# Kernel optimization log

Measured on AMD Instinct MI355X. Metric: run time of the kernel, lower is better.

Reference implementation:

```python
import jax, jax.numpy as jnp
import numpy as np

B, N, D, H, K, FFN = 8, 256, 512, 16, 4, 2048
DK = D // H
NEG = -1e12


def _lin(k, i, o):
    return jax.random.normal(k, (i, o), jnp.float32) / np.sqrt(i)


def setup_inputs() -> dict:
    key = jax.random.key(0)
    ks = jax.random.split(key, 12)
    return {
        "x": jax.random.normal(ks[0], (B, N, D), jnp.float32),
        "dist": jax.random.uniform(ks[1], (B, N - 1, N - 1), jnp.float32) * 10.0,
        "dist_bar": jnp.array([1.5, 3.0, 5.0, 8.0], jnp.float32),
        "attn_bias": 0.1 * jax.random.normal(ks[2], (B, K, N, N), jnp.float32),
        "mask": jnp.ones((B, 1, N, N), jnp.int32),
        "num_heads": H,
        "Wq": _lin(ks[3], D, D), "bq": jnp.zeros((D,), jnp.float32),
        "Wk": _lin(ks[4], D, D), "bk": jnp.zeros((D,), jnp.float32),
        "Wv": _lin(ks[5], D, D), "bv": jnp.zeros((D,), jnp.float32),
        "W1": _lin(ks[6], K * D, D), "b1": jnp.zeros((D,), jnp.float32),
        "W2": _lin(ks[7], D, D), "b2": jnp.zeros((D,), jnp.float32),
        "g1": jnp.ones((D,), jnp.float32), "be1": jnp.zeros((D,), jnp.float32),
        "Wf1": _lin(ks[8], D, FFN), "bf1": jnp.zeros((FFN,), jnp.float32),
        "Wf2": _lin(ks[9], FFN, D), "bf2": jnp.zeros((D,), jnp.float32),
        "g2": jnp.ones((D,), jnp.float32), "be2": jnp.zeros((D,), jnp.float32),
    }


def _ln(x, g, b, eps=1e-6):
    m = jnp.mean(x, -1, keepdims=True)
    v = jnp.mean((x - m) ** 2, -1, keepdims=True)
    return (x - m) / jnp.sqrt(v + eps) * g + b


def _forward(x, dist, dist_bar, attn_bias, mask, num_heads,
             Wq, bq, Wk, bk, Wv, bv, W1, b1, W2, b2, g1, be1,
             Wf1, bf1, Wf2, bf2, g2, be2):
    Bn, Nn, Dn = x.shape
    Hh = num_heads
    dk = Dn // Hh
    Kk = dist_bar.shape[0]

    q = (x @ Wq + bq).reshape(Bn, Nn, Hh, dk).transpose(0, 2, 1, 3)  # [B,H,N,dk]
    k = (x @ Wk + bk).reshape(Bn, Nn, Hh, dk).transpose(0, 2, 1, 3)
    v = (x @ Wv + bv).reshape(Bn, Nn, Hh, dk).transpose(0, 2, 1, 3)

    scores = jnp.einsum('bhnd,bhmd->bhnm', q, k) / np.sqrt(dk)      # [B,H,N,N]
    # expand over scales and add bias: [B,H,K,N,N]
    scores = scores[:, :, None, :, :] + attn_bias[:, None, :, :, :]
    # padding mask [B,1,N,N] -> broadcast over H,K
    scores = jnp.where(mask[:, None] == 0, NEG, scores)

    # build padded distance with super node (row/col 0 distance = 0)
    nd = jnp.ones((Bn, Nn, Nn), x.dtype)
    nd = nd.at[:, 1:, 1:].set(dist)
    nd = nd.at[:, 0, :].set(0.0).at[:, :, 0].set(0.0)
    masks = nd[:, None, None, :, :] < dist_bar.reshape(1, 1, Kk, 1, 1)  # [B,1,K,N,N]
    masks = masks.at[:, :, :, 0, :].set(True).at[:, :, :, :, 0].set(True)

    scores = jnp.where(masks, scores, NEG)
    attn = jax.nn.softmax(scores, axis=-1)                           # [B,H,K,N,N]

    msg = jnp.einsum('bhknm,bhmd->bhknd', attn, v)                   # [B,H,K,N,dk]
    # faithful to torch: transpose(1,2).view(B,H*K,N,dk) then transpose(2,3).view(B,N,-1)
    msg = jnp.transpose(msg, (0, 2, 1, 3, 4)).reshape(Bn, Kk * Hh, Nn, dk)
    msg = jnp.transpose(msg, (0, 1, 3, 2)).reshape(Bn, Nn, Kk * Hh * dk)

    h = jax.nn.silu(msg @ W1 + b1) @ W2 + b2
    y = _ln(h + x, g1, be1)

    f = jax.nn.gelu(y @ Wf1 + bf1, approximate=False) @ Wf2 + bf2
    out = _ln(f + y, g2, be2)
    return out


def reference(x, dist, dist_bar, attn_bias, mask, num_heads,
              Wq, bq, Wk, bk, Wv, bv, W1, b1, W2, b2, g1, be1,
              Wf1, bf1, Wf2, bf2, g2, be2):
    return _forward(x, dist, dist_bar, attn_bias, mask, num_heads,
                    Wq, bq, Wk, bk, Wv, bv, W1, b1, W2, b2, g1, be1,
                    Wf1, bf1, Wf2, bf2, g2, be2)
```

## Files before the change

### kernel.cpp

```cpp
#include <hip/hip_runtime.h>
#include <math.h>

#define BB 8
#define NN 256
#define DD 512
#define HH 16
#define KK 4
#define DKK 32
#define FFN_ 2048
#define NEGV -1e12f

typedef __attribute__((ext_vector_type(8))) short bf16x8;
typedef __attribute__((ext_vector_type(4))) float f32x4;

__device__ __forceinline__ unsigned short f2bf(float f) {
    union { float f; unsigned int u; } v; v.f = f;
    unsigned int r = (v.u + 0x7FFFu + ((v.u >> 16) & 1u)) >> 16;
    return (unsigned short)r;
}
__device__ __forceinline__ float bf2f(unsigned short u) {
    union { unsigned int i; float f; } v; v.i = ((unsigned int)u) << 16;
    return v.f;
}
__device__ __forceinline__ void gload_lds16(const unsigned short* g, unsigned short* l) {
    __builtin_amdgcn_global_load_lds(
        (const __attribute__((address_space(1))) void*)g,
        (__attribute__((address_space(3))) void*)l, 16, 0, 0);
}

__global__ __launch_bounds__(256) void prep_kernel(
    const float* __restrict__ x,
    const float* __restrict__ Wq, const float* __restrict__ Wk,
    const float* __restrict__ Wv, const float* __restrict__ W1,
    const float* __restrict__ W2, const float* __restrict__ Wf1,
    const float* __restrict__ Wf2,
    const float* __restrict__ bq, const float* __restrict__ bk,
    const float* __restrict__ bv,
    const float* __restrict__ attn_bias, const int* __restrict__ mask,
    const float* __restrict__ dist, const float* __restrict__ dist_bar,
    unsigned short* __restrict__ xb, unsigned short* __restrict__ Wqkvt,
    unsigned short* __restrict__ W1t, unsigned short* __restrict__ W2t,
    unsigned short* __restrict__ Wf1t, unsigned short* __restrict__ Wf2t,
    float* __restrict__ bqkv, unsigned short* __restrict__ biasMs)
{
    const int z = blockIdx.z;
    const int t = threadIdx.x;

    if (z == 7) {
        if (blockIdx.x >= 1024) return;
        const int i0 = blockIdx.x * 1024 + t * 4;
        float4 xv = *(const float4*)(x + i0);
        ushort4 o;
        o.x = f2bf(xv.x); o.y = f2bf(xv.y); o.z = f2bf(xv.z); o.w = f2bf(xv.w);
        *(ushort4*)(xb + i0) = o;
        return;
    }
    if (z == 8) {
        if (blockIdx.x >= 6) return;
        const int i = blockIdx.x * 256 + t;
        float v = (i < 512) ? bq[i] : (i < 1024) ? bk[i - 512] : bv[i - 1024];
        bqkv[i] = v;
        return;
    }
    if (z == 9) {
        const int bx = blockIdx.x;
        const int rg = bx & 63, ks = (bx >> 6) & 3, b = bx >> 8;
        const int m = t;
        const float bar = dist_bar[ks];
        ushort4 o;
        unsigned short* po = (unsigned short*)&o;
        #pragma unroll
        for (int i = 0; i < 4; ++i) {
            const int n = rg * 4 + i;
            const int mk = mask[((size_t)(b * NN) + n) * NN + m];
            bool allowed = (n == 0) || (m == 0);
            if (!allowed)
                allowed = dist[((size_t)(b * 255) + (n - 1)) * 255 + (m - 1)] < bar;
            const float bias = attn_bias[(((size_t)(b * KK) + ks) * NN + n) * NN + m];
            po[i] = f2bf((mk != 0 && allowed) ? bias : NEGV);
        }
        *(ushort4*)(biasMs + (size_t)bx * 1024 + m * 4) = o;
        return;
    }

    const float* src; unsigned short* dst; int Kd, Nd;
    switch (z) {
        case 0: src = Wq;  dst = Wqkvt;              Kd = 512;  Nd = 512;  break;
        case 1: src = Wk;  dst = Wqkvt + 512 * 512;  Kd = 512;  Nd = 512;  break;
        case 2: src = Wv;  dst = Wqkvt + 1024 * 512; Kd = 512;  Nd = 512;  break;
        case 3: src = W1;  dst = W1t;  Kd = 2048; Nd = 512;  break;
        case 4: src = W2;  dst = W2t;  Kd = 512;  Nd = 512;  break;
        case 5: src = Wf1; dst = Wf1t; Kd = 512;  Nd = 2048; break;
        default: src = Wf2; dst = Wf2t; Kd = 2048; Nd = 512; break;
    }
    const int ktiles = Kd / 32, ntiles = Nd / 32;
    const int ti = blockIdx.x;
    if (ti >= ktiles * ntiles) return;
    const int k0 = (ti % ktiles) * 32, n0 = (ti / ktiles) * 32;

    __shared__ float tile[32][33];
    const int xx = t & 31, yy = t >> 5;
    #pragma unroll
    for (int r = 0; r < 4; ++r)
        tile[yy * 4 + r][xx] = src[(size_t)(k0 + yy * 4 + r) * Nd + n0 + xx];
    __syncthreads();
    #pragma unroll
    for (int r = 0; r < 4; ++r)
        dst[(size_t)(n0 + yy * 4 + r) * Kd + k0 + xx] = f2bf(tile[xx][yy * 4 + r]);
}

template<int ACT, int EPI, int KSPLIT>
__global__ __launch_bounds__(512) void mfma_gemm512(
    const unsigned short* __restrict__ A, const unsigned short* __restrict__ Bt,
    const float* __restrict__ bias, unsigned short* __restrict__ Cb,
    unsigned short* __restrict__ vT, float* __restrict__ Cp,
    int M, int N, int Kdim)
{
    __shared__ unsigned short As[128 * 64];
    __shared__ unsigned short Bs[128 * 64];

    const int t = threadIdx.x, lane = t & 63, wv = t >> 6;
    const int n0 = blockIdx.x * 128, m0 = blockIdx.y * 128;
    const int wm = wv >> 1, wn = wv & 1;
    const int L = lane & 15, qd = lane >> 4;
    const int sr = lane >> 3, sc = lane & 7;

    const int ksub = Kdim / KSPLIT;
    const int kbeg = blockIdx.z * ksub;

    f32x4 acc[2][4];
    #pragma unroll
    for (int i = 0; i < 2; ++i)
        #pragma unroll
        for (int j = 0; j < 4; ++j) acc[i][j] = (f32x4){0.f, 0.f, 0.f, 0.f};

    for (int kt = kbeg; kt < kbeg + ksub; kt += 64) {
        #pragma unroll
        for (int p = 0; p < 2; ++p) {
            const int rbase = wv * 16 + p * 8;
            gload_lds16(A  + (size_t)(m0 + rbase + sr) * Kdim + kt + sc * 8,
                        As + rbase * 64);
            gload_lds16(Bt + (size_t)(n0 + rbase + sr) * Kdim + kt + sc * 8,
                        Bs + rbase * 64);
        }
        __syncthreads();
        #pragma unroll
        for (int s = 0; s < 2; ++s) {
            bf16x8 af[2], bfb[4];
            #pragma unroll
            for (int i = 0; i < 2; ++i)
                af[i] = *(const bf16x8*)(As + (wm * 32 + i * 16 + L) * 64 + s * 32 + qd * 8);
            #pragma unroll
            for (int j = 0; j < 4; ++j)
                bfb[j] = *(const bf16x8*)(Bs + (wn * 64 + j * 16 + L) * 64 + s * 32 + qd * 8);
            #pragma unroll
            for (int i = 0; i < 2; ++i)
                #pragma unroll
                for (int j = 0; j < 4; ++j)
                    acc[i][j] = __builtin_amdgcn_mfma_f32_16x16x32_bf16(af[i], bfb[j], acc[i][j], 0, 0, 0);
        }
        __syncthreads();
    }

    #pragma unroll
    for (int j = 0; j < 4; ++j) {
        const int col = n0 + wn * 64 + j * 16 + L;
        #pragma unroll
        for (int i = 0; i < 2; ++i) {
            const int rowb = m0 + wm * 32 + i * 16 + qd * 4;
            if (EPI == 2) {
                float* cp = Cp + (size_t)blockIdx.z * M * N + (size_t)rowb * N + col;
                #pragma unroll
                for (int r = 0; r < 4; ++r) cp[(size_t)r * N] = acc[i][j][r];
            } else if (EPI == 1 && col >= 1024) {
                const float bv = bias[col];
                ushort4 pk;
                unsigned short* pp = (unsigned short*)&pk;
                #pragma unroll
                for (int r = 0; r < 4; ++r) pp[r] = f2bf(acc[i][j][r] + bv);
                *(ushort4*)(vT + (size_t)(col - 1024) * 2048 + rowb) = pk;
            } else {
                const float bv = bias[col];
                #pragma unroll
                for (int r = 0; r < 4; ++r) {
                    float v = acc[i][j][r] + bv;
                    if (ACT == 1) v = v / (1.0f + __expf(-v));
                    else if (ACT == 2) v = 0.5f * v * (1.0f + erff(v * 0.70710678118654752f));
                    Cb[(size_t)(rowb + r) * N + col] = f2bf(v);
                }
            }
        }
    }
}

__global__ __launch_bounds__(256) void fin_silu(
    const float* __restrict__ Cp, const float* __restrict__ bias,
    unsigned short* __restrict__ out)
{
    const int row = blockIdx.x, t = threadIdx.x;
    const int c0 = t * 2;
    const size_t base = (size_t)row * DD;
    float sx = 0.f, sy = 0.f;
    #pragma unroll
    for (int z = 0; z < 4; ++z) {
        const float2 p = *(const float2*)(Cp + (size_t)z * (2048u * 512u) + base + c0);
        sx += p.x; sy += p.y;
    }
    float v0 = sx + bias[c0], v1 = sy + bias[c0 + 1];
    v0 = v0 / (1.0f + __expf(-v0));
    v1 = v1 / (1.0f + __expf(-v1));
    ushort2 pk; pk.x = f2bf(v0); pk.y = f2bf(v1);
    *(ushort2*)(out + base + c0) = pk;
}

template<int KS, int OUT16>
__global__ __launch_bounds__(256) void fin_ln(
    const float* __restrict__ Cp, const float* __restrict__ bias,
    const float* __restrict__ res, const float* __restrict__ g,
    const float* __restrict__ be, float* __restrict__ out,
    unsigned short* __restrict__ outb)
{
    const int row = blockIdx.x, t = threadIdx.x;
    const int c0 = t * 2;
    const size_t base = (size_t)row * DD;
    __shared__ float red[256];

    float sx = 0.f, sy = 0.f;
    #pragma unroll
    for (int z = 0; z < KS; ++z) {
        const float2 p = *(const float2*)(Cp + (size_t)z * (2048u * 512u) + base + c0);
        sx += p.x; sy += p.y;
    }
    const float2 rv = *(const float2*)(res + base + c0);
    const float z0 = sx + bias[c0]     + rv.x;
    const float z1 = sy + bias[c0 + 1] + rv.y;

    red[t] = z0 + z1; __syncthreads();
    for (int s = 128; s > 0; s >>= 1) {
        if (t < s) red[t] += red[t + s];
        __syncthreads();
    }
    const float mean = red[0] * (1.0f / 512.0f); __syncthreads();

    const float d0 = z0 - mean, d1 = z1 - mean;
    red[t] = d0 * d0 + d1 * d1; __syncthreads();
    for (int s = 128; s > 0; s >>= 1) {
        if (t < s) red[t] += red[t + s];
        __syncthreads();
    }
    const float inv = rsqrtf(red[0] * (1.0f / 512.0f) + 1e-6f);

    const float o0 = d0 * inv * g[c0]     + be[c0];
    const float o1 = d1 * inv * g[c0 + 1] + be[c0 + 1];
    out[base + c0]     = o0;
    out[base + c0 + 1] = o1;
    if (OUT16) {
        ushort2 pk; pk.x = f2bf(o0); pk.y = f2bf(o1);
        *(ushort2*)(outb + base + c0) = pk;
    }
}

__global__ __launch_bounds__(256) void attn_kernel(
    const unsigned short* __restrict__ qkvb, const unsigned short* __restrict__ vT,
    const unsigned short* __restrict__ biasMs, unsigned short* __restrict__ msgT)
{
    const int qt = blockIdx.x, h = blockIdx.y, b = blockIdx.z;
    const int q0 = qt * 64;
    const int t = threadIdx.x, lane = t & 63, wv = t >> 6;
    const int L = lane & 15, qd = lane >> 4;

    __shared__ unsigned short Qs[64 * 32];
    __shared__ unsigned short Ks[256 * 32];
    __shared__ unsigned short Vs[32 * 264];
    __shared__ unsigned short Ps[64 * 264];
    __shared__ unsigned short Ot[32 * 72];

    {
        const int r = lane >> 2, c = lane & 3;
        gload_lds16(qkvb + (size_t)(b * NN + q0 + wv * 16 + r) * 1536 + h * DKK + c * 8,
                    Qs + wv * 16 * 32);
        #pragma unroll
        for (int p = 0; p < 4; ++p)
            gload_lds16(qkvb + (size_t)(b * NN + p * 64 + wv * 16 + r) * 1536 + 512 + h * DKK + c * 8,
                        Ks + (p * 64 + wv * 16) * 32);
    }
    {
        const int vr = t >> 3, seg = t & 7;
        const unsigned short* gv = vT + (size_t)(h * DKK + vr) * 2048 + b * NN + seg * 32;
        #pragma unroll
        for (int i = 0; i < 4; ++i) {
            bf16x8 vv = *(const bf16x8*)(gv + i * 8);
            *(bf16x8*)(Vs + vr * 264 + seg * 32 + i * 8) = vv;
        }
    }
    __syncthreads();

    f32x4 S[16];
    #pragma unroll
    for (int j = 0; j < 16; ++j) S[j] = (f32x4){0.f, 0.f, 0.f, 0.f};
    {
        const bf16x8 aq = *(const bf16x8*)(Qs + (wv * 16 + L) * 32 + qd * 8);
        #pragma unroll
        for (int j = 0; j < 16; ++j) {
            const bf16x8 bk = *(const bf16x8*)(Ks + (j * 16 + L) * 32 + qd * 8);
            S[j] = __builtin_amdgcn_mfma_f32_16x16x32_bf16(aq, bk, S[j], 0, 0, 0);
        }
    }
    const float scale = 0.17677669529663687f;
    const int rgb = (q0 + wv * 16) >> 2;

    for (int ks = 0; ks < KK; ++ks) {
        const unsigned short* bp = biasMs + ((size_t)((b * KK + ks) * 64 + rgb + qd)) * 1024;

        ushort4 b4[16];
        float mx[4] = {-3e38f, -3e38f, -3e38f, -3e38f};
        #pragma unroll
        for (int j = 0; j < 16; ++j) {
            b4[j] = *(const ushort4*)(bp + (j * 16 + L) * 4);
            const unsigned short* pb = (const unsigned short*)&b4[j];
            #pragma unroll
            for (int r = 0; r < 4; ++r)
                mx[r] = fmaxf(mx[r], S[j][r] * scale + bf2f(pb[r]));
        }
        #pragma unroll
        for (int off = 8; off > 0; off >>= 1)
            #pragma unroll
            for (int r = 0; r < 4; ++r)
                mx[r] = fmaxf(mx[r], __shfl_xor(mx[r], off));

        float sm[4] = {0.f, 0.f, 0.f, 0.f};
        #pragma unroll
        for (int j = 0; j < 16; ++j) {
            const unsigned short* pb = (const unsigned short*)&b4[j];
            #pragma unroll
            for (int r = 0; r < 4; ++r) {
                const float e = __expf(S[j][r] * scale + bf2f(pb[r]) - mx[r]);
                sm[r] += e;
                Ps[(wv * 16 + qd * 4 + r) * 264 + j * 16 + L] = f2bf(e);
            }
        }
        #pragma unroll
        for (int off = 8; off > 0; off >>= 1)
            #pragma unroll
            for (int r = 0; r < 4; ++r)
                sm[r] += __shfl_xor(sm[r], off);
        float inv[4];
        #pragma unroll
        for (int r = 0; r < 4; ++r) inv[r] = 1.0f / sm[r];

        f32x4 O[2];
        O[0] = (f32x4){0.f, 0.f, 0.f, 0.f};
        O[1] = (f32x4){0.f, 0.f, 0.f, 0.f};
        #pragma unroll
        for (int kc = 0; kc < 8; ++kc) {
            const bf16x8 ap = *(const bf16x8*)(Ps + (wv * 16 + L) * 264 + kc * 32 + qd * 8);
            #pragma unroll
            for (int jt = 0; jt < 2; ++jt) {
                const bf16x8 bv = *(const bf16x8*)(Vs + (jt * 16 + L) * 264 + kc * 32 + qd * 8);
                O[jt] = __builtin_amdgcn_mfma_f32_16x16x32_bf16(ap, bv, O[jt], 0, 0, 0);
            }
        }
        #pragma unroll
        for (int jt = 0; jt < 2; ++jt)
            #pragma unroll
            for (int r = 0; r < 4; ++r)
                Ot[(jt * 16 + L) * 72 + wv * 16 + qd * 4 + r] = f2bf(O[jt][r] * inv[r]);
        __syncthreads();

        {
            const int dd = t >> 3, cc = t & 7;
            bf16x8 ov = *(const bf16x8*)(Ot + dd * 72 + cc * 8);
            *(bf16x8*)(msgT + (size_t)b * 524288 +
                       ((size_t)((ks * HH + h) * DKK + dd)) * NN + q0 + cc * 8) = ov;
        }
        __syncthreads();
    }
}

extern "C" void kernel_launch(void* const* d_in, const int* in_sizes, int n_in,
                              void* d_out, int out_size, void* d_ws, size_t ws_size,
                              hipStream_t stream)
{
    const float* x         = (const float*)d_in[0];
    const float* dist      = (const float*)d_in[1];
    const float* dist_bar  = (const float*)d_in[2];
    const float* attn_bias = (const float*)d_in[3];
    const int*   mask      = (const int*)d_in[4];
    const float* Wq  = (const float*)d_in[6];  const float* bq  = (const float*)d_in[7];
    const float* Wk  = (const float*)d_in[8];  const float* bk  = (const float*)d_in[9];
    const float* Wv  = (const float*)d_in[10]; const float* bv  = (const float*)d_in[11];
    const float* W1  = (const float*)d_in[12]; const float* b1  = (const float*)d_in[13];
    const float* W2  = (const float*)d_in[14]; const float* b2  = (const float*)d_in[15];
    const float* g1  = (const float*)d_in[16]; const float* be1 = (const float*)d_in[17];
    const float* Wf1 = (const float*)d_in[18]; const float* bf1 = (const float*)d_in[19];
    const float* Wf2 = (const float*)d_in[20]; const float* bf2 = (const float*)d_in[21];
    const float* g2  = (const float*)d_in[22]; const float* be2 = (const float*)d_in[23];

    float* ws = (float*)d_ws;
    unsigned short* qkvb   = (unsigned short*)(ws + 0);
    unsigned short* vT     = (unsigned short*)(ws + 1572864);
    unsigned short* xb     = (unsigned short*)(ws + 2097152);
    unsigned short* msgT   = (unsigned short*)(ws + 2621440);
    unsigned short* g3     = msgT;
    unsigned short* biasMs = (unsigned short*)(ws + 4718592);
    float*          bqkv   = ws + 5767168;
    unsigned short* h1     = (unsigned short*)(ws + 5771264);
    float*          yb     = ws + 6295552;
    unsigned short* yb16   = (unsigned short*)(ws + 7344128);
    unsigned short* Wqkvt  = (unsigned short*)(ws + 7868416);
    unsigned short* W1t    = (unsigned short*)(ws + 8261632);
    unsigned short* W2t    = (unsigned short*)(ws + 8785920);
    unsigned short* Wf1t   = (unsigned short*)(ws + 8916992);
    unsigned short* Wf2t   = (unsigned short*)(ws + 9441280);
    float*          part   = ws + 9965568;
    float*          outp   = (float*)d_out;

    const int M = BB * NN;

    prep_kernel<<<dim3(2048, 1, 10), dim3(256), 0, stream>>>(
        x, Wq, Wk, Wv, W1, W2, Wf1, Wf2, bq, bk, bv,
        attn_bias, mask, dist, dist_bar,
        xb, Wqkvt, W1t, W2t, Wf1t, Wf2t, bqkv, biasMs);

    mfma_gemm512<0,1,1><<<dim3(12, 16, 1), dim3(512), 0, stream>>>(
        xb, Wqkvt, bqkv, qkvb, vT, nullptr, M, 1536, DD);

    attn_kernel<<<dim3(4, HH, BB), dim3(256), 0, stream>>>(qkvb, vT, biasMs, msgT);

    mfma_gemm512<0,2,4><<<dim3(4, 16, 4), dim3(512), 0, stream>>>(
        msgT, W1t, nullptr, nullptr, nullptr, part, M, DD, 2048);
    fin_silu<<<dim3(M), dim3(256), 0, stream>>>(part, b1, h1);

    mfma_gemm512<0,2,2><<<dim3(4, 16, 2), dim3(512), 0, stream>>>(
        h1, W2t, nullptr, nullptr, nullptr, part, M, DD, DD);
    fin_ln<2,1><<<dim3(M), dim3(256), 0, stream>>>(part, b2, x, g1, be1, yb, yb16);

    mfma_gemm512<2,0,1><<<dim3(16, 16, 1), dim3(512), 0, stream>>>(
        yb16, Wf1t, bf1, g3, nullptr, nullptr, M, FFN_, DD);

    mfma_gemm512<0,2,4><<<dim3(4, 16, 4), dim3(512), 0, stream>>>(
        g3, Wf2t, nullptr, nullptr, nullptr, part, M, DD, 2048);
    fin_ln<4,0><<<dim3(M), dim3(256), 0, stream>>>(part, bf2, yb, g2, be2, outp, nullptr);
}
```

Baseline: 254.0 us.

## Fuse all stages into one cooperative persistent kernel with grid syncs

Replaces the chain of ten separate kernel launches with a single cooperative mega-kernel of 256 blocks that runs prep, QKV GEMM, attention, the MLP GEMMs and layer norms as stages separated by grid.sync. Split-K partial buffers and finalize kernels are removed: GEMMs now use 64x64 tiles with fused bias/activation epilogues, and layer norm becomes a wave-per-row shuffle reduction. Attention is restructured so each block handles half the queries of one (batch, head), with per-wave scratch. The aim is to cut launch overhead and partial-sum traffic, at the cost of low parallelism in some stages (256 blocks, long-K GEMMs with small tiles) and grid-wide barrier costs.

Result: slower. 529.2 us (+108.3%).

```diff
diff --git a/kernel.cpp b/kernel.cpp
--- a/kernel.cpp
+++ b/kernel.cpp
@@ -1,5 +1,8 @@
 #include <hip/hip_runtime.h>
+#include <hip/hip_cooperative_groups.h>
 #include <math.h>
+
+namespace cg = cooperative_groups;
 
 #define BB 8
 #define NN 256
@@ -28,7 +31,7 @@
         (__attribute__((address_space(3))) void*)l, 16, 0, 0);
 }
 
-__global__ __launch_bounds__(256) void prep_kernel(
+__device__ void prep_stage(
     const float* __restrict__ x,
     const float* __restrict__ Wq, const float* __restrict__ Wk,
     const float* __restrict__ Wv, const float* __restrict__ W1,
@@ -41,92 +44,83 @@
     unsigned short* __restrict__ xb, unsigned short* __restrict__ Wqkvt,
     unsigned short* __restrict__ W1t, unsigned short* __restrict__ W2t,
     unsigned short* __restrict__ Wf1t, unsigned short* __restrict__ Wf2t,
-    float* __restrict__ bqkv, unsigned short* __restrict__ biasMs)
-{
-    const int z = blockIdx.z;
+    float* __restrict__ bqkv, unsigned short* __restrict__ biasMs, char* lds)
+{
+    float* tile = (float*)lds;
     const int t = threadIdx.x;
 
-    if (z == 7) {
-        if (blockIdx.x >= 1024) return;
-        const int i0 = blockIdx.x * 1024 + t * 4;
-        float4 xv = *(const float4*)(x + i0);
-        ushort4 o;
-        o.x = f2bf(xv.x); o.y = f2bf(xv.y); o.z = f2bf(xv.z); o.w = f2bf(xv.w);
-        *(ushort4*)(xb + i0) = o;
-        return;
-    }
-    if (z == 8) {
-        if (blockIdx.x >= 6) return;
-        const int i = blockIdx.x * 256 + t;
-        float v = (i < 512) ? bq[i] : (i < 1024) ? bk[i - 512] : bv[i - 1024];
-        bqkv[i] = v;
-        return;
-    }
-    if (z == 9) {
-        const int bx = blockIdx.x;
-        const int rg = bx & 63, ks = (bx >> 6) & 3, b = bx >> 8;
-        const int m = t;
-        const float bar = dist_bar[ks];
-        ushort4 o;
-        unsigned short* po = (unsigned short*)&o;
-        #pragma unroll
-        for (int i = 0; i < 4; ++i) {
-            const int n = rg * 4 + i;
-            const int mk = mask[((size_t)(b * NN) + n) * NN + m];
-            bool allowed = (n == 0) || (m == 0);
-            if (!allowed)
-                allowed = dist[((size_t)(b * 255) + (n - 1)) * 255 + (m - 1)] < bar;
-            const float bias = attn_bias[(((size_t)(b * KK) + ks) * NN + n) * NN + m];
-            po[i] = f2bf((mk != 0 && allowed) ? bias : NEGV);
-        }
-        *(ushort4*)(biasMs + (size_t)bx * 1024 + m * 4) = o;
-        return;
-    }
-
-    const float* src; unsigned short* dst; int Kd, Nd;
-    switch (z) {
-        case 0: src = Wq;  dst = Wqkvt;              Kd = 512;  Nd = 512;  break;
-        case 1: src = Wk;  dst = Wqkvt + 512 * 512;  Kd = 512;  Nd = 512;  break;
-        case 2: src = Wv;  dst = Wqkvt + 1024 * 512; Kd = 512;  Nd = 512;  break;
-        case 3: src = W1;  dst = W1t;  Kd = 2048; Nd = 512;  break;
-        case 4: src = W2;  dst = W2t;  Kd = 512;  Nd = 512;  break;
-        case 5: src = Wf1; dst = Wf1t; Kd = 512;  Nd = 2048; break;
-        default: src = Wf2; dst = Wf2t; Kd = 2048; Nd = 512; break;
-    }
-    const int ktiles = Kd / 32, ntiles = Nd / 32;
-    const int ti = blockIdx.x;
-    if (ti >= ktiles * ntiles) return;
-    const int k0 = (ti % ktiles) * 32, n0 = (ti / ktiles) * 32;
-
-    __shared__ float tile[32][33];
-    const int xx = t & 31, yy = t >> 5;
-    #pragma unroll
-    for (int r = 0; r < 4; ++r)
-        tile[yy * 4 + r][xx] = src[(size_t)(k0 + yy * 4 + r) * Nd + n0 + xx];
-    __syncthreads();
-    #pragma unroll
-    for (int r = 0; r < 4; ++r)
-        dst[(size_t)(n0 + yy * 4 + r) * Kd + k0 + xx] = f2bf(tile[xx][yy * 4 + r]);
-}
-
-template<int ACT, int EPI, int KSPLIT>
-__global__ __launch_bounds__(512) void mfma_gemm512(
-    const unsigned short* __restrict__ A, const unsigned short* __restrict__ Bt,
-    const float* __restrict__ bias, unsigned short* __restrict__ Cb,
-    unsigned short* __restrict__ vT, float* __restrict__ Cp,
-    int M, int N, int Kdim)
-{
-    __shared__ unsigned short As[128 * 64];
-    __shared__ unsigned short Bs[128 * 64];
-
+    for (int job = blockIdx.x; job < 5379; job += 256) {
+        if (job < 4096) {
+            const float* src; unsigned short* dst; int Kd, Nd, ti;
+            if (job < 768) {
+                const int w = job >> 8; ti = job & 255;
+                src = (w == 0) ? Wq : (w == 1) ? Wk : Wv;
+                dst = Wqkvt + w * 262144; Kd = 512; Nd = 512;
+            } else if (job < 1792) { src = W1;  dst = W1t;  Kd = 2048; Nd = 512;  ti = job - 768; }
+            else if (job < 2048)   { src = W2;  dst = W2t;  Kd = 512;  Nd = 512;  ti = job - 1792; }
+            else if (job < 3072)   { src = Wf1; dst = Wf1t; Kd = 512;  Nd = 2048; ti = job - 2048; }
+            else                   { src = Wf2; dst = Wf2t; Kd = 2048; Nd = 512;  ti = job - 3072; }
+            const int kt = Kd >> 5;
+            const int k0 = (ti % kt) * 32, n0 = (ti / kt) * 32;
+            const int xx = t & 31, yy = t >> 5;
+            __syncthreads();
+            #pragma unroll
+            for (int rr = 0; rr < 2; ++rr)
+                tile[(yy * 2 + rr) * 33 + xx] = src[(size_t)(k0 + yy * 2 + rr) * Nd + n0 + xx];
+            __syncthreads();
+            #pragma unroll
+            for (int rr = 0; rr < 2; ++rr)
+                dst[(size_t)(n0 + yy * 2 + rr) * Kd + k0 + xx] = f2bf(tile[xx * 33 + yy * 2 + rr]);
+        } else if (job < 4352) {
+            const int j = job - 4096;
+            const size_t i0 = (size_t)j * 4096 + t * 8;
+            const float4 a = *(const float4*)(x + i0);
+            const float4 c = *(const float4*)(x + i0 + 4);
+            unsigned short o[8] = {f2bf(a.x), f2bf(a.y), f2bf(a.z), f2bf(a.w),
+                                   f2bf(c.x), f2bf(c.y), f2bf(c.z), f2bf(c.w)};
+            *(bf16x8*)(xb + i0) = *(bf16x8*)o;
+        } else if (job < 5376) {
+            const int j = job - 4352;
+            const int b = j >> 7, ks = (j >> 5) & 3, rgp = j & 31;
+            const int rg = rgp * 2 + (t >> 8), m = t & 255;
+            const int bx = (b * 4 + ks) * 64 + rg;
+            const float bar = dist_bar[ks];
+            ushort4 o; unsigned short* po = (unsigned short*)&o;
+            #pragma unroll
+            for (int i = 0; i < 4; ++i) {
+                const int n = rg * 4 + i;
+                const int mk = mask[((size_t)(b * NN) + n) * NN + m];
+                bool allowed = (n == 0) || (m == 0);
+                if (!allowed)
+                    allowed = dist[((size_t)(b * 255) + (n - 1)) * 255 + (m - 1)] < bar;
+                const float bias = attn_bias[(((size_t)(b * KK) + ks) * NN + n) * NN + m];
+                po[i] = f2bf((mk != 0 && allowed) ? bias : NEGV);
+            }
+            *(ushort4*)(biasMs + (size_t)bx * 1024 + m * 4) = o;
+        } else {
+            const int j = job - 5376;
+            const int i = j * 512 + t;
+            bqkv[i] = (i < 512) ? bq[i] : (i < 1024) ? bk[i - 512] : bv[i - 1024];
+        }
+    }
+}
+
+template<int ACT, int QKV>
+__device__ void gemm128(const unsigned short* __restrict__ A,
+                        const unsigned short* __restrict__ Bt,
+                        const float* __restrict__ bias,
+                        unsigned short* __restrict__ Cb,
+                        unsigned short* __restrict__ vTo,
+                        int N, int Kdim, int njobs, int ntile, char* lds)
+{
+    unsigned short* As = (unsigned short*)lds;
+    unsigned short* Bs = As + 8192;
     const int t = threadIdx.x, lane = t & 63, wv = t >> 6;
-    const int n0 = blockIdx.x * 128, m0 = blockIdx.y * 128;
     const int wm = wv >> 1, wn = wv & 1;
     const int L = lane & 15, qd = lane >> 4;
-    const int sr = lane >> 3, sc = lane & 7;
-
-    const int ksub = Kdim / KSPLIT;
-    const int kbeg = blockIdx.z * ksub;
+    const int job = blockIdx.x;
+    if (job >= njobs) return;
+    const int n0 = (job % ntile) * 128, m0 = (job / ntile) * 128;
 
     f32x4 acc[2][4];
     #pragma unroll
@@ -134,14 +128,13 @@
         #pragma unroll
         for (int j = 0; j < 4; ++j) acc[i][j] = (f32x4){0.f, 0.f, 0.f, 0.f};
 
-    for (int kt = kbeg; kt < kbeg + ksub; kt += 64) {
-        #pragma unroll
-        for (int p = 0; p < 2; ++p) {
-            const int rbase = wv * 16 + p * 8;
-            gload_lds16(A  + (size_t)(m0 + rbase + sr) * Kdim + kt + sc * 8,
-                        As + rbase * 64);
-            gload_lds16(Bt + (size_t)(n0 + rbase + sr) * Kdim + kt + sc * 8,
-                        Bs + rbase * 64);
+    for (int kt = 0; kt < Kdim; kt += 64) {
+        #pragma unroll
+        for (int i = 0; i < 2; ++i) {
+            gload_lds16(A  + (size_t)(m0 + wv * 16 + i * 8 + (lane >> 3)) * Kdim + kt + (lane & 7) * 8,
+                        As + (wv * 16 + i * 8) * 64);
+            gload_lds16(Bt + (size_t)(n0 + wv * 16 + i * 8 + (lane >> 3)) * Kdim + kt + (lane & 7) * 8,
+                        Bs + (wv * 16 + i * 8) * 64);
         }
         __syncthreads();
         #pragma unroll
@@ -165,27 +158,20 @@
     #pragma unroll
     for (int j = 0; j < 4; ++j) {
         const int col = n0 + wn * 64 + j * 16 + L;
+        const float bv = bias[col];
         #pragma unroll
         for (int i = 0; i < 2; ++i) {
             const int rowb = m0 + wm * 32 + i * 16 + qd * 4;
-            if (EPI == 2) {
-                float* cp = Cp + (size_t)blockIdx.z * M * N + (size_t)rowb * N + col;
-                #pragma unroll
-                for (int r = 0; r < 4; ++r) cp[(size_t)r * N] = acc[i][j][r];
-            } else if (EPI == 1 && col >= 1024) {
-                const float bv = bias[col];
-                ushort4 pk;
-                unsigned short* pp = (unsigned short*)&pk;
+            if (QKV == 1 && col >= 1024) {
+                ushort4 pk; unsigned short* pp = (unsigned short*)&pk;
                 #pragma unroll
                 for (int r = 0; r < 4; ++r) pp[r] = f2bf(acc[i][j][r] + bv);
-                *(ushort4*)(vT + (size_t)(col - 1024) * 2048 + rowb) = pk;
+                *(ushort4*)(vTo + (size_t)(col - 1024) * 2048 + rowb) = pk;
             } else {
-                const float bv = bias[col];
                 #pragma unroll
                 for (int r = 0; r < 4; ++r) {
                     float v = acc[i][j][r] + bv;
-                    if (ACT == 1) v = v / (1.0f + __expf(-v));
-                    else if (ACT == 2) v = 0.5f * v * (1.0f + erff(v * 0.70710678118654752f));
+                    if (ACT == 2) v = 0.5f * v * (1.0f + erff(v * 0.70710678118654752f));
                     Cb[(size_t)(rowb + r) * N + col] = f2bf(v);
                 }
             }
@@ -193,105 +179,77 @@
     }
 }
 
-__global__ __launch_bounds__(256) void fin_silu(
-    const float* __restrict__ Cp, const float* __restrict__ bias,
-    unsigned short* __restrict__ out)
-{
-    const int row = blockIdx.x, t = threadIdx.x;
-    const int c0 = t * 2;
-    const size_t base = (size_t)row * DD;
-    float sx = 0.f, sy = 0.f;
-    #pragma unroll
-    for (int z = 0; z < 4; ++z) {
-        const float2 p = *(const float2*)(Cp + (size_t)z * (2048u * 512u) + base + c0);
-        sx += p.x; sy += p.y;
-    }
-    float v0 = sx + bias[c0], v1 = sy + bias[c0 + 1];
-    v0 = v0 / (1.0f + __expf(-v0));
-    v1 = v1 / (1.0f + __expf(-v1));
-    ushort2 pk; pk.x = f2bf(v0); pk.y = f2bf(v1);
-    *(ushort2*)(out + base + c0) = pk;
-}
-
-template<int KS, int OUT16>
-__global__ __launch_bounds__(256) void fin_ln(
-    const float* __restrict__ Cp, const float* __restrict__ bias,
-    const float* __restrict__ res, const float* __restrict__ g,
-    const float* __restrict__ be, float* __restrict__ out,
-    unsigned short* __restrict__ outb)
-{
-    const int row = blockIdx.x, t = threadIdx.x;
-    const int c0 = t * 2;
-    const size_t base = (size_t)row * DD;
-    __shared__ float red[256];
-
-    float sx = 0.f, sy = 0.f;
-    #pragma unroll
-    for (int z = 0; z < KS; ++z) {
-        const float2 p = *(const float2*)(Cp + (size_t)z * (2048u * 512u) + base + c0);
-        sx += p.x; sy += p.y;
-    }
-    const float2 rv = *(const float2*)(res + base + c0);
-    const float z0 = sx + bias[c0]     + rv.x;
-    const float z1 = sy + bias[c0 + 1] + rv.y;
-
-    red[t] = z0 + z1; __syncthreads();
-    for (int s = 128; s > 0; s >>= 1) {
-        if (t < s) red[t] += red[t + s];
+template<int ACT, int OUTF32>
+__device__ void gemm64(const unsigned short* __restrict__ A,
+                       const unsigned short* __restrict__ Bt,
+                       const float* __restrict__ bias,
+                       unsigned short* __restrict__ Cb, float* __restrict__ Cf,
+                       int N, int Kdim, char* lds)
+{
+    unsigned short* As = (unsigned short*)lds;
+    unsigned short* Bs = As + 4096;
+    const int t = threadIdx.x, lane = t & 63, wv = t >> 6;
+    const int wm = wv >> 1, wn = wv & 1;
+    const int L = lane & 15, qd = lane >> 4;
+    const int ntile = N >> 6;
+    const int job = blockIdx.x;
+    const int n0 = (job & (ntile - 1)) * 64, m0 = (job / ntile) * 64;
+
+    f32x4 acc[2] = {(f32x4){0.f,0.f,0.f,0.f}, (f32x4){0.f,0.f,0.f,0.f}};
+
+    for (int kt = 0; kt < Kdim; kt += 64) {
+        gload_lds16(A  + (size_t)(m0 + wv * 8 + (lane >> 3)) * Kdim + kt + (lane & 7) * 8,
+                    As + wv * 8 * 64);
+        gload_lds16(Bt + (size_t)(n0 + wv * 8 + (lane >> 3)) * Kdim + kt + (lane & 7) * 8,
+                    Bs + wv * 8 * 64);
         __syncthreads();
-    }
-    const float mean = red[0] * (1.0f / 512.0f); __syncthreads();
-
-    const float d0 = z0 - mean, d1 = z1 - mean;
-    red[t] = d0 * d0 + d1 * d1; __syncthreads();
-    for (int s = 128; s > 0; s >>= 1) {
-        if (t < s) red[t] += red[t + s];
+        #pragma unroll
+        for (int s = 0; s < 2; ++s) {
+            const bf16x8 a = *(const bf16x8*)(As + (wm * 16 + L) * 64 + s * 32 + qd * 8);
+            #pragma unroll
+            for (int j = 0; j < 2; ++j) {
+                const bf16x8 b = *(const bf16x8*)(Bs + (wn * 32 + j * 16 + L) * 64 + s * 32 + qd * 8);
+                acc[j] = __builtin_amdgcn_mfma_f32_16x16x32_bf16(a, b, acc[j], 0, 0, 0);
+            }
+        }
         __syncthreads();
     }
-    const float inv = rsqrtf(red[0] * (1.0f / 512.0f) + 1e-6f);
-
-    const float o0 = d0 * inv * g[c0]     + be[c0];
-    const float o1 = d1 * inv * g[c0 + 1] + be[c0 + 1];
-    out[base + c0]     = o0;
-    out[base + c0 + 1] = o1;
-    if (OUT16) {
-        ushort2 pk; pk.x = f2bf(o0); pk.y = f2bf(o1);
-        *(ushort2*)(outb + base + c0) = pk;
-    }
-}
-
-__global__ __launch_bounds__(256) void attn_kernel(
-    const unsigned short* __restrict__ qkvb, const unsigned short* __restrict__ vT,
-    const unsigned short* __restrict__ biasMs, unsigned short* __restrict__ msgT)
-{
-    const int qt = blockIdx.x, h = blockIdx.y, b = blockIdx.z;
-    const int q0 = qt * 64;
+
+    #pragma unroll
+    for (int j = 0; j < 2; ++j) {
+        const int col = n0 + wn * 32 + j * 16 + L;
+        const float bv = bias[col];
+        #pragma unroll
+        for (int r = 0; r < 4; ++r) {
+            const int row = m0 + wm * 16 + qd * 4 + r;
+            float v = acc[j][r] + bv;
+            if (ACT == 1) v = v / (1.0f + __expf(-v));
+            if (OUTF32) Cf[(size_t)row * N + col] = v;
+            else        Cb[(size_t)row * N + col] = f2bf(v);
+        }
+    }
+}
+
+__device__ void attn_stage(const unsigned short* __restrict__ qkvb,
+                           const unsigned short* __restrict__ vTb,
+                           const unsigned short* __restrict__ biasMs,
+                           unsigned short* __restrict__ msgT, char* lds)
+{
+    const int bid = blockIdx.x;
+    const int b = bid >> 5, h = (bid >> 1) & 15, qh = bid & 1;
     const int t = threadIdx.x, lane = t & 63, wv = t >> 6;
     const int L = lane & 15, qd = lane >> 4;
-
-    __shared__ unsigned short Qs[64 * 32];
-    __shared__ unsigned short Ks[256 * 32];
-    __shared__ unsigned short Vs[32 * 264];
-    __shared__ unsigned short Ps[64 * 264];
-    __shared__ unsigned short Ot[32 * 72];
+    const int qbase = qh * 128 + wv * 16;
+
+    unsigned short* Vs  = (unsigned short*)lds;
+    unsigned short* Pch = (unsigned short*)(lds + 16896) + wv * 640;
+    unsigned short* Ot  = (unsigned short*)(lds + 27136) + wv * 768;
 
     {
-        const int r = lane >> 2, c = lane & 3;
-        gload_lds16(qkvb + (size_t)(b * NN + q0 + wv * 16 + r) * 1536 + h * DKK + c * 8,
-                    Qs + wv * 16 * 32);
-        #pragma unroll
-        for (int p = 0; p < 4; ++p)
-            gload_lds16(qkvb + (size_t)(b * NN + p * 64 + wv * 16 + r) * 1536 + 512 + h * DKK + c * 8,
-                        Ks + (p * 64 + wv * 16) * 32);
-    }
-    {
-        const int vr = t >> 3, seg = t & 7;
-        const unsigned short* gv = vT + (size_t)(h * DKK + vr) * 2048 + b * NN + seg * 32;
-        #pragma unroll
-        for (int i = 0; i < 4; ++i) {
-            bf16x8 vv = *(const bf16x8*)(gv + i * 8);
-            *(bf16x8*)(Vs + vr * 264 + seg * 32 + i * 8) = vv;
-        }
+        const int d = t >> 4, seg = t & 15;
+        const unsigned short* gv = vTb + (size_t)(h * DKK + d) * 2048 + b * NN + seg * 16;
+        *(bf16x8*)(Vs + d * 264 + seg * 16)     = *(const bf16x8*)(gv);
+        *(bf16x8*)(Vs + d * 264 + seg * 16 + 8) = *(const bf16x8*)(gv + 8);
     }
     __syncthreads();
 
@@ -299,15 +257,19 @@
     #pragma unroll
     for (int j = 0; j < 16; ++j) S[j] = (f32x4){0.f, 0.f, 0.f, 0.f};
     {
-        const bf16x8 aq = *(const bf16x8*)(Qs + (wv * 16 + L) * 32 + qd * 8);
+        const bf16x8 aq = *(const bf16x8*)(qkvb + (size_t)(b * NN + qbase + L) * 1536 + h * DKK + qd * 8);
         #pragma unroll
         for (int j = 0; j < 16; ++j) {
-            const bf16x8 bk = *(const bf16x8*)(Ks + (j * 16 + L) * 32 + qd * 8);
+            const bf16x8 bk = *(const bf16x8*)(qkvb + (size_t)(b * NN + j * 16 + L) * 1536 + 512 + h * DKK + qd * 8);
             S[j] = __builtin_amdgcn_mfma_f32_16x16x32_bf16(aq, bk, S[j], 0, 0, 0);
         }
     }
     const float scale = 0.17677669529663687f;
-    const int rgb = (q0 + wv * 16) >> 2;
+    #pragma unroll
+    for (int j = 0; j < 16; ++j)
+        #pragma unroll
+        for (int r = 0; r < 4; ++r) S[j][r] *= scale;
+    const int rgb = qbase >> 2;
 
     for (int ks = 0; ks < KK; ++ks) {
         const unsigned short* bp = biasMs + ((size_t)((b * KK + ks) * 64 + rgb + qd)) * 1024;
@@ -320,30 +282,30 @@
             const unsigned short* pb = (const unsigned short*)&b4[j];
             #pragma unroll
             for (int r = 0; r < 4; ++r)
-                mx[r] = fmaxf(mx[r], S[j][r] * scale + bf2f(pb[r]));
+                mx[r] = fmaxf(mx[r], S[j][r] + bf2f(pb[r]));
         }
         #pragma unroll
         for (int off = 8; off > 0; off >>= 1)
             #pragma unroll
-            for (int r = 0; r < 4; ++r)
-                mx[r] = fmaxf(mx[r], __shfl_xor(mx[r], off));
-
+            for (int r = 0; r < 4; ++r) mx[r] = fmaxf(mx[r], __shfl_xor(mx[r], off));
+
+        ushort4 e16[16];
         float sm[4] = {0.f, 0.f, 0.f, 0.f};
         #pragma unroll
         for (int j = 0; j < 16; ++j) {
             const unsigned short* pb = (const unsigned short*)&b4[j];
+            unsigned short* pe = (unsigned short*)&e16[j];
             #pragma unroll
             for (int r = 0; r < 4; ++r) {
-                const float e = __expf(S[j][r] * scale + bf2f(pb[r]) - mx[r]);
+                const float e = __expf(S[j][r] + bf2f(pb[r]) - mx[r]);
                 sm[r] += e;
-                Ps[(wv * 16 + qd * 4 + r) * 264 + j * 16 + L] = f2bf(e);
+                pe[r] = f2bf(e);
             }
         }
         #pragma unroll
         for (int off = 8; off > 0; off >>= 1)
             #pragma unroll
-            for (int r = 0; r < 4; ++r)
-                sm[r] += __shfl_xor(sm[r], off);
+            for (int r = 0; r < 4; ++r) sm[r] += __shfl_xor(sm[r], off);
         float inv[4];
         #pragma unroll
         for (int r = 0; r < 4; ++r) inv[r] = 1.0f / sm[r];
@@ -353,28 +315,125 @@
         O[1] = (f32x4){0.f, 0.f, 0.f, 0.f};
         #pragma unroll
         for (int kc = 0; kc < 8; ++kc) {
-            const bf16x8 ap = *(const bf16x8*)(Ps + (wv * 16 + L) * 264 + kc * 32 + qd * 8);
+            #pragma unroll
+            for (int j2 = 0; j2 < 2; ++j2) {
+                const unsigned short* pe = (const unsigned short*)&e16[kc * 2 + j2];
+                #pragma unroll
+                for (int r = 0; r < 4; ++r)
+                    Pch[(qd * 4 + r) * 40 + j2 * 16 + L] = pe[r];
+            }
+            asm volatile("s_waitcnt lgkmcnt(0)" ::: "memory");
+            const bf16x8 ap = *(const bf16x8*)(Pch + L * 40 + qd * 8);
             #pragma unroll
             for (int jt = 0; jt < 2; ++jt) {
                 const bf16x8 bv = *(const bf16x8*)(Vs + (jt * 16 + L) * 264 + kc * 32 + qd * 8);
                 O[jt] = __builtin_amdgcn_mfma_f32_16x16x32_bf16(ap, bv, O[jt], 0, 0, 0);
             }
         }
+
         #pragma unroll
         for (int jt = 0; jt < 2; ++jt)
             #pragma unroll
             for (int r = 0; r < 4; ++r)
-                Ot[(jt * 16 + L) * 72 + wv * 16 + qd * 4 + r] = f2bf(O[jt][r] * inv[r]);
-        __syncthreads();
-
+                Ot[(jt * 16 + L) * 24 + qd * 4 + r] = f2bf(O[jt][r] * inv[r]);
+        asm volatile("s_waitcnt lgkmcnt(0)" ::: "memory");
         {
-            const int dd = t >> 3, cc = t & 7;
-            bf16x8 ov = *(const bf16x8*)(Ot + dd * 72 + cc * 8);
+            const int d = lane >> 1, qp = lane & 1;
+            const bf16x8 ov = *(const bf16x8*)(Ot + d * 24 + qp * 8);
             *(bf16x8*)(msgT + (size_t)b * 524288 +
-                       ((size_t)((ks * HH + h) * DKK + dd)) * NN + q0 + cc * 8) = ov;
-        }
-        __syncthreads();
-    }
+                       ((size_t)((ks * HH + h) * DKK + d)) * 256 + qbase + qp * 8) = ov;
+        }
+    }
+}
+
+template<int OUT16>
+__device__ void ln_stage(const float* __restrict__ a, const float* __restrict__ r,
+                         const float* __restrict__ g, const float* __restrict__ be,
+                         float* __restrict__ out, unsigned short* __restrict__ outb)
+{
+    const int t = threadIdx.x, lane = t & 63, wv = t >> 6;
+    const int row = blockIdx.x * 8 + wv;
+    const size_t base = (size_t)row * DD + lane * 8;
+    const int c0 = lane * 8;
+
+    float z[8]; float s = 0.f;
+    #pragma unroll
+    for (int i = 0; i < 8; ++i) { z[i] = a[base + i] + r[base + i]; s += z[i]; }
+    #pragma unroll
+    for (int off = 32; off > 0; off >>= 1) s += __shfl_xor(s, off);
+    const float mean = s * (1.0f / 512.0f);
+    float v = 0.f;
+    #pragma unroll
+    for (int i = 0; i < 8; ++i) { z[i] -= mean; v += z[i] * z[i]; }
+    #pragma unroll
+    for (int off = 32; off > 0; off >>= 1) v += __shfl_xor(v, off);
+    const float inv = rsqrtf(v * (1.0f / 512.0f) + 1e-6f);
+
+    unsigned short o16[8];
+    #pragma unroll
+    for (int i = 0; i < 8; ++i) {
+        const float o = z[i] * inv * g[c0 + i] + be[c0 + i];
+        out[base + i] = o;
+        if (OUT16) o16[i] = f2bf(o);
+    }
+    if (OUT16) *(bf16x8*)(outb + base) = *(bf16x8*)o16;
+}
+
+__global__ __launch_bounds__(512, 2) void mega_kernel(
+    const float* __restrict__ x, const float* __restrict__ dist,
+    const float* __restrict__ dist_bar, const float* __restrict__ attn_bias,
+    const int* __restrict__ mask,
+    const float* __restrict__ Wq, const float* __restrict__ bq,
+    const float* __restrict__ Wk, const float* __restrict__ bk,
+    const float* __restrict__ Wv, const float* __restrict__ bv,
+    const float* __restrict__ W1, const float* __restrict__ b1,
+    const float* __restrict__ W2, const float* __restrict__ b2,
+    const float* __restrict__ g1, const float* __restrict__ be1,
+    const float* __restrict__ Wf1, const float* __restrict__ bf1,
+    const float* __restrict__ Wf2, const float* __restrict__ bf2,
+    const float* __restrict__ g2, const float* __restrict__ be2,
+    float* __restrict__ ws, float* __restrict__ outp)
+{
+    __shared__ __align__(16) char smem[39424];
+    cg::grid_group grid = cg::this_grid();
+
+    unsigned short* qkvb   = (unsigned short*)(ws + 0);
+    unsigned short* vT     = (unsigned short*)(ws + 1572864);
+    unsigned short* xb     = (unsigned short*)(ws + 2097152);
+    unsigned short* msgT   = (unsigned short*)(ws + 2621440);
+    unsigned short* biasMs = (unsigned short*)(ws + 4718592);
+    float*          bqkv   = ws + 5767168;
+    unsigned short* h1     = (unsigned short*)(ws + 5771264);
+    float*          h2     = ws + 6295552;
+    float*          yb     = ws + 7344128;
+    unsigned short* yb16   = (unsigned short*)(ws + 8392704);
+    unsigned short* g3     = (unsigned short*)(ws + 8916992);
+    float*          fb     = ws + 11014144;
+    unsigned short* Wqkvt  = (unsigned short*)(ws + 12062720);
+    unsigned short* W1t    = (unsigned short*)(ws + 12455936);
+    unsigned short* W2t    = (unsigned short*)(ws + 12980224);
+    unsigned short* Wf1t   = (unsigned short*)(ws + 13111296);
+    unsigned short* Wf2t   = (unsigned short*)(ws + 13635584);
+
+    prep_stage(x, Wq, Wk, Wv, W1, W2, Wf1, Wf2, bq, bk, bv,
+               attn_bias, mask, dist, dist_bar,
+               xb, Wqkvt, W1t, W2t, Wf1t, Wf2t, bqkv, biasMs, smem);
+    grid.sync();
+    gemm128<0, 1>(xb, Wqkvt, bqkv, qkvb, vT, 1536, DD, 192, 12, smem);
+    grid.sync();
+    attn_stage(qkvb, vT, biasMs, msgT, smem);
+    grid.sync();
+    gemm64<1, 0>(msgT, W1t, b1, h1, nullptr, DD, 2048, smem);
+    grid.sync();
+    gemm64<0, 1>(h1, W2t, b2, nullptr, h2, DD, DD, smem);
+    grid.sync();
+    ln_stage<1>(h2, x, g1, be1, yb, yb16);
+    grid.sync();
+    gemm128<2, 0>(yb16, Wf1t, bf1, g3, nullptr, FFN_, DD, 256, 16, smem);
+    grid.sync();
+    gemm64<0, 1>(g3, Wf2t, bf2, nullptr, fb, DD, 2048, smem);
+    grid.sync();
+    ln_stage<0>(fb, yb, g2, be2, outp, nullptr);
 }
 
 extern "C" void kernel_launch(void* const* d_in, const int* in_sizes, int n_in,
@@ -396,49 +455,16 @@
     const float* Wf2 = (const float*)d_in[20]; const float* bf2 = (const float*)d_in[21];
     const float* g2  = (const float*)d_in[22]; const float* be2 = (const float*)d_in[23];
 
-    float* ws = (float*)d_ws;
-    unsigned short* qkvb   = (unsigned short*)(ws + 0);
-    unsigned short* vT     = (unsigned short*)(ws + 1572864);
-    unsigned short* xb     = (unsigned short*)(ws + 2097152);
-    unsigned short* msgT   = (unsigned short*)(ws + 2621440);
-    unsigned short* g3     = msgT;
-    unsigned short* biasMs = (unsigned short*)(ws + 4718592);
-    float*          bqkv   = ws + 5767168;
-    unsigned short* h1     = (unsigned short*)(ws + 5771264);
-    float*          yb     = ws + 6295552;
-    unsigned short* yb16   = (unsigned short*)(ws + 7344128);
-    unsigned short* Wqkvt  = (unsigned short*)(ws + 7868416);
-    unsigned short* W1t    = (unsigned short*)(ws + 8261632);
-    unsigned short* W2t    = (unsigned short*)(ws + 8785920);
-    unsigned short* Wf1t   = (unsigned short*)(ws + 8916992);
-    unsigned short* Wf2t   = (unsigned short*)(ws + 9441280);
-    float*          part   = ws + 9965568;
-    float*          outp   = (float*)d_out;
-
-    const int M = BB * NN;
-
-    prep_kernel<<<dim3(2048, 1, 10), dim3(256), 0, stream>>>(
-        x, Wq, Wk, Wv, W1, W2, Wf1, Wf2, bq, bk, bv,
-        attn_bias, mask, dist, dist_bar,
-        xb, Wqkvt, W1t, W2t, Wf1t, Wf2t, bqkv, biasMs);
-
-    mfma_gemm512<0,1,1><<<dim3(12, 16, 1), dim3(512), 0, stream>>>(
-        xb, Wqkvt, bqkv, qkvb, vT, nullptr, M, 1536, DD);
-
-    attn_kernel<<<dim3(4, HH, BB), dim3(256), 0, stream>>>(qkvb, vT, biasMs, msgT);
-
-    mfma_gemm512<0,2,4><<<dim3(4, 16, 4), dim3(512), 0, stream>>>(
-        msgT, W1t, nullptr, nullptr, nullptr, part, M, DD, 2048);
-    fin_silu<<<dim3(M), dim3(256), 0, stream>>>(part, b1, h1);
-
-    mfma_gemm512<0,2,2><<<dim3(4, 16, 2), dim3(512), 0, stream>>>(
-        h1, W2t, nullptr, nullptr, nullptr, part, M, DD, DD);
-    fin_ln<2,1><<<dim3(M), dim3(256), 0, stream>>>(part, b2, x, g1, be1, yb, yb16);
-
-    mfma_gemm512<2,0,1><<<dim3(16, 16, 1), dim3(512), 0, stream>>>(
-        yb16, Wf1t, bf1, g3, nullptr, nullptr, M, FFN_, DD);
-
-    mfma_gemm512<0,2,4><<<dim3(4, 16, 4), dim3(512), 0, stream>>>(
-        g3, Wf2t, nullptr, nullptr, nullptr, part, M, DD, 2048);
-    fin_ln<4,0><<<dim3(M), dim3(256), 0, stream>>>(part, bf2, yb, g2, be2, outp, nullptr);
-}
+    float* wsp  = (float*)d_ws;
+    float* outp = (float*)d_out;
+
+    void* kargs[] = {
+        (void*)&x, (void*)&dist, (void*)&dist_bar, (void*)&attn_bias, (void*)&mask,
+        (void*)&Wq, (void*)&bq, (void*)&Wk, (void*)&bk, (void*)&Wv, (void*)&bv,
+        (void*)&W1, (void*)&b1, (void*)&W2, (void*)&b2, (void*)&g1, (void*)&be1,
+        (void*)&Wf1, (void*)&bf1, (void*)&Wf2, (void*)&bf2, (void*)&g2, (void*)&be2,
+        (void*)&wsp, (void*)&outp
+    };
+    hipLaunchCooperativeKernel((const void*)mega_kernel, dim3(256), dim3(512),
+                               kargs, 0, stream);
+}
```
